# Kernel tuning notes

Measured on AMD Instinct MI355X. Metric: run time of the kernel, lower is better.

Reference implementation:

```python
import jax, jax.numpy as jnp
import numpy as np

H = 16          # head_num
DH = 64         # h_size = all_head_size // head_num
HIDDEN = 1024
ALL_HEAD = 1024
B, S = 4, 2048
NEG = -1000000000.0


def setup_inputs() -> dict:
    key = jax.random.key(0)
    ks = jax.random.split(key, 8)
    x = jax.random.normal(ks[0], (B, S, HIDDEN), dtype=jnp.float32)
    y = jax.random.normal(ks[1], (B, S, HIDDEN), dtype=jnp.float32)
    attention_mask = jax.random.randint(ks[2], (B, 1, S, S), 0, 2, dtype=jnp.int32)
    sc = 1.0 / np.sqrt(HIDDEN)
    Wq = jax.random.normal(ks[3], (HIDDEN, ALL_HEAD), dtype=jnp.float32) * sc
    Wk = jax.random.normal(ks[4], (HIDDEN, ALL_HEAD), dtype=jnp.float32) * sc
    Wv = jax.random.normal(ks[5], (HIDDEN, ALL_HEAD), dtype=jnp.float32) * sc
    Wo = jax.random.normal(ks[6], (ALL_HEAD, HIDDEN), dtype=jnp.float32) * (1.0 / np.sqrt(ALL_HEAD))
    bo = jnp.zeros((HIDDEN,), dtype=jnp.float32)
    return {"x": x, "y": y, "Wq": Wq, "Wk": Wk, "Wv": Wv, "Wo": Wo, "bo": bo,
            "attention_mask": attention_mask}


def reference(x, y, Wq, Wk, Wv, Wo, bo, attention_mask):
    b = x.shape[0]
    # projections, split heads: [B, H, S, Dh]
    q = (x @ Wq).reshape(b, -1, H, DH).transpose(0, 2, 1, 3)
    k = (x @ Wk).reshape(b, -1, H, DH).transpose(0, 2, 1, 3)
    v = (y @ Wv).reshape(b, -1, H, DH).transpose(0, 2, 1, 3)
    mask = attention_mask == 0  # True => masked (matches .eq(0))
    scores = jnp.einsum('bhqd,bhkd->bhqk', q, k)
    scores = jnp.where(mask, NEG, scores)  # masked_fill BEFORE scaling, as in source
    attn = jax.nn.softmax(scores / np.sqrt(DH), axis=-1)
    ctx = jnp.einsum('bhqk,bhkd->bhqd', attn, v)
    ctx = ctx.transpose(0, 2, 1, 3).reshape(b, -1, H * DH)
    return ctx @ Wo + bo  # dropout p=0.0 is identity
```

## Files before the change

### kernel.cpp

```cpp
#include <hip/hip_runtime.h>
#include <hip/hip_bf16.h>
#include <stdint.h>

typedef __attribute__((ext_vector_type(8))) short short8;
typedef __attribute__((ext_vector_type(4))) float f32x4;
typedef __attribute__((ext_vector_type(16))) float f32x16;
typedef __hip_bfloat16 bf16;

typedef __attribute__((address_space(3))) uint32_t lds_u32_t;
typedef __attribute__((address_space(1))) const uint32_t glb_u32_t;

__device__ __forceinline__ void gload_lds16(const void* g, void* l) {
  __builtin_amdgcn_global_load_lds((glb_u32_t*)g, (lds_u32_t*)l, 16, 0, 0);
}

__device__ __forceinline__ uint32_t cvt_pk_bf16(float lo, float hi_) {
  uint32_t r;
  asm volatile("v_cvt_pk_bf16_f32 %0, %1, %2" : "=v"(r) : "v"(lo), "v"(hi_));
  return r;
}

__device__ __forceinline__ void plane32swap(uint32_t &a, uint32_t &b) {
  auto r = __builtin_amdgcn_permlane32_swap((int)a, (int)b, false, false);
  a = (uint32_t)r[0]; b = (uint32_t)r[1];
}


__global__ void conv_bf16(const float* __restrict__ in, bf16* __restrict__ outp, int n4) {
  int i = blockIdx.x * blockDim.x + threadIdx.x;
  if (i >= n4) return;
  const float4 v = ((const float4*)in)[i];
  union { ushort4 u; bf16 h[4]; } o;
  o.h[0] = __float2bfloat16(v.x); o.h[1] = __float2bfloat16(v.y);
  o.h[2] = __float2bfloat16(v.z); o.h[3] = __float2bfloat16(v.w);
  ((ushort4*)outp)[i] = o.u;
}

__global__ void transpose_w(const float* __restrict__ W0, const float* __restrict__ W1,
                            const float* __restrict__ W2, const float* __restrict__ W3,
                            bf16* __restrict__ outp) {
  const float* W = blockIdx.z == 0 ? W0 : blockIdx.z == 1 ? W1 : blockIdx.z == 2 ? W2 : W3;
  bf16* o = outp + (size_t)blockIdx.z * 1048576;
  __shared__ float t[32][33];
  int x = threadIdx.x, y0 = threadIdx.y;
  int c0 = blockIdx.x * 32, r0 = blockIdx.y * 32;
#pragma unroll
  for (int i = 0; i < 4; i++)
    t[y0 + i*8][x] = W[(size_t)(r0 + y0 + i*8)*1024 + c0 + x];
  __syncthreads();
#pragma unroll
  for (int i = 0; i < 4; i++)
    o[(size_t)(c0 + y0 + i*8)*1024 + r0 + x] = __float2bfloat16(t[x][y0 + i*8]);
}

__global__ void maskpack(const int* __restrict__ mask, unsigned long long* __restrict__ mbits) {
  int tid = threadIdx.x;
  int lane = tid & 63, wid = tid >> 6;
  size_t word = (size_t)blockIdx.x * 4 + wid;
  int v = mask[word * 64 + lane];
  unsigned long long bits = __ballot(v == 0);
  if (lane == 0) mbits[word] = bits;
}

template<int MODE>
__global__ void gemm_bt(const bf16* __restrict__ A, const bf16* __restrict__ Bt,
                        void* __restrict__ Out, const float* __restrict__ bias) {
  const int tid = threadIdx.x;
  const int lane = tid & 63, wid = tid >> 6;
  const int g = lane >> 4, c = lane & 15;
  const int m0 = blockIdx.x * 128, n0 = blockIdx.y * 128;
  const int wm = wid >> 1, wn = wid & 1;
  __shared__ bf16 As[128 * 64];
  __shared__ bf16 Bs[128 * 64];
  f32x4 acc[4][4] = {};
  for (int k0 = 0; k0 < 1024; k0 += 64) {
#pragma unroll
    for (int i = 0; i < 4; i++) {
      int chunk = wid * 4 + i;
      int idx = chunk * 64 + lane;
      int row = idx >> 3, u = idx & 7;
      int koff = k0 + ((u ^ (row & 7)) * 8);
      gload_lds16(A  + (size_t)(m0 + row) * 1024 + koff, As + chunk * 512);
      gload_lds16(Bt + (size_t)(n0 + row) * 1024 + koff, Bs + chunk * 512);
    }
    __syncthreads();
#pragma unroll
    for (int kk = 0; kk < 2; kk++) {
      short8 af[4], bf_[4];
#pragma unroll
      for (int f = 0; f < 4; f++) {
        int ra = wm * 64 + f * 16 + c;
        af[f]  = *(const short8*)(As + ra * 64 + (((kk * 4 + g) ^ (ra & 7)) * 8));
        int rb = wn * 64 + f * 16 + c;
        bf_[f] = *(const short8*)(Bs + rb * 64 + (((kk * 4 + g) ^ (rb & 7)) * 8));
      }
#pragma unroll
      for (int fm = 0; fm < 4; fm++)
#pragma unroll
        for (int fn = 0; fn < 4; fn++)
          acc[fm][fn] = __builtin_amdgcn_mfma_f32_16x16x32_bf16(af[fm], bf_[fn], acc[fm][fn], 0, 0, 0);
    }
    __syncthreads();
  }
#pragma unroll
  for (int fm = 0; fm < 4; fm++) {
#pragma unroll
    for (int fn = 0; fn < 4; fn++) {
      int gn = n0 + wn * 64 + fn * 16 + c;
#pragma unroll
      for (int r = 0; r < 4; r++) {
        int gm = m0 + wm * 64 + fm * 16 + g * 4 + r;
        float v = acc[fm][fn][r];
        if constexpr (MODE == 2) {
          ((float*)Out)[(size_t)gm * 1024 + gn] = v + bias[gn];
        } else if constexpr (MODE == 0) {
          int b = gm >> 11, s = gm & 2047, hh = gn >> 6, d = gn & 63;
          ((bf16*)Out)[(((size_t)b * 16 + hh) * 2048 + s) * 64 + d] = __float2bfloat16(v);
        } else {
          int b = gm >> 11, s = gm & 2047, hh = gn >> 6, d = gn & 63;
          ((bf16*)Out)[(((size_t)b * 16 + hh) * 64 + d) * 2048 + s] = __float2bfloat16(v);
        }
      }
    }
  }
}

__global__ __launch_bounds__(256, 4) void attn_kernel(
    const bf16* __restrict__ Qb, const bf16* __restrict__ Kb, const bf16* __restrict__ Vt,
    const unsigned long long* __restrict__ mbits, bf16* __restrict__ ctx) {
  const int tid = threadIdx.x;
  const int lane = tid & 63, wid = tid >> 6;
  const int c5 = lane & 31, hi = lane >> 5;
  const int sid = blockIdx.x;
  const int xcd = sid & 7, idx = sid >> 3;
  const int bh = xcd * 8 + (idx >> 4);
  const int qb0 = (idx & 15) * 128 + wid * 32;
  const int b = bh >> 4, h = bh & 15;
  __shared__ bf16 Ks[2][64 * 64];
  __shared__ bf16 Vs[3][64 * 64];
  const bf16* Qp = Qb + (size_t)bh * 2048 * 64;
  const bf16* Kp = Kb + (size_t)bh * 2048 * 64;
  const bf16* Vp = Vt + (size_t)bh * 64 * 2048;
  const unsigned long long* mrow = mbits + ((size_t)b * 2048 + qb0 + c5) * 32;

  auto stage_k = [&](int kt, int sk) {
#pragma unroll
    for (int i = 0; i < 2; i++) {
      int chunk = wid * 2 + i;
      int idx2 = chunk * 64 + lane;
      int row = idx2 >> 3, u = idx2 & 7;
      gload_lds16(Kp + (size_t)(kt * 64 + row) * 64 + ((u ^ (row & 7)) * 8), &Ks[sk][chunk * 512]);
    }
  };
  auto stage_v = [&](int kt, int sv) {
#pragma unroll
    for (int i = 0; i < 2; i++) {
      int chunk = wid * 2 + i;
      int idx2 = chunk * 64 + lane;
      int row = idx2 >> 3, u = idx2 & 7;
      gload_lds16(Vp + (size_t)row * 2048 + kt * 64 + ((u ^ (row & 7)) * 8), &Vs[sv][chunk * 512]);
    }
  };

  short8 qf[4];
#pragma unroll
  for (int ks = 0; ks < 4; ks++)
    qf[ks] = *(const short8*)(Qp + (size_t)(qb0 + c5) * 64 + ks * 16 + hi * 8);

  f32x16 Oacc0 = {}, Oacc1 = {};
  float mrun = -3.0e38f, mc1 = 0.f, lrun = 0.f;
  short8 paP[4];

  const float C1 = 0.18033688011112042f;
  const float THRRAW = 44.36f;

  unsigned long long mwC, mwN;
  stage_k(0, 0);
  stage_v(0, 0);
  mwC = mrow[0];
  __syncthreads();

  int sv = 0, svp = 2;
  for (int kt = 0; kt < 32; kt++) {
    const int sk = kt & 1;
    const int svn = (sv == 2) ? 0 : sv + 1;
    if (kt < 31) { stage_k(kt + 1, sk ^ 1); stage_v(kt + 1, svn); }
    mwN = mrow[(kt + 1) & 31];

    f32x16 s0 = {}, s1 = {};
    __builtin_amdgcn_s_setprio(1);
#pragma unroll
    for (int ks = 0; ks < 4; ks++) {
      short8 aK0 = *(const short8*)(&Ks[sk][(c5)      * 64 + (((ks * 2 + hi) ^ (c5 & 7)) * 8)]);
      short8 aK1 = *(const short8*)(&Ks[sk][(32 + c5) * 64 + (((ks * 2 + hi) ^ (c5 & 7)) * 8)]);
      s0 = __builtin_amdgcn_mfma_f32_32x32x16_bf16(aK0, qf[ks], s0, 0, 0, 0);
      s1 = __builtin_amdgcn_mfma_f32_32x32x16_bf16(aK1, qf[ks], s1, 0, 0, 0);
    }
    if (kt > 0) {
#pragma unroll
      for (int ks = 0; ks < 4; ks++) {
        short8 bV0 = *(const short8*)(&Vs[svp][(c5)      * 64 + (((ks * 2 + hi) ^ (c5 & 7)) * 8)]);
        short8 bV1 = *(const short8*)(&Vs[svp][(32 + c5) * 64 + (((ks * 2 + hi) ^ (c5 & 7)) * 8)]);
        Oacc0 = __builtin_amdgcn_mfma_f32_32x32x16_bf16(paP[ks], bV0, Oacc0, 0, 0, 0);
        Oacc1 = __builtin_amdgcn_mfma_f32_32x32x16_bf16(paP[ks], bV1, Oacc1, 0, 0, 0);
      }
    }
    __builtin_amdgcn_s_setprio(0);
    float lmx = fmaxf(s0[0], s1[0]);
#pragma unroll
    for (int reg = 1; reg < 16; reg++)
      lmx = fmaxf(fmaxf(s0[reg], s1[reg]), lmx);
    if (__any(lmx > mrun + THRRAW)) {
      float rmx = fmaxf(lmx, __shfl_xor(lmx, 32));
      float mnew = fmaxf(mrun, rmx);
      float sc = exp2f((mrun - mnew) * C1);
      mrun = mnew; mc1 = mnew * C1;
      lrun *= sc;
#pragma unroll
      for (int reg = 0; reg < 16; reg++) {
        const int qrow = (reg & 3) + 8 * (reg >> 2) + 4 * hi;
        float srow = __shfl(sc, qrow);
        Oacc0[reg] *= srow; Oacc1[reg] *= srow;
      }
    }
    const uint32_t nlo = ~(((uint32_t)mwC)         >> (4 * hi));
    const uint32_t nhi = ~(((uint32_t)(mwC >> 32)) >> (4 * hi));
    uint32_t pk0[8], pk1[8];
    float lsum = 0.f;
#pragma unroll
    for (int r8 = 0; r8 < 8; r8++) {
      const int rA = 2 * r8, rB = 2 * r8 + 1;
      const int pA = (rA & 3) + 8 * (rA >> 2), pB = (rB & 3) + 8 * (rB >> 2);
      float a0 = exp2f(fmaf(s0[rA], C1, -mc1));
      float a1 = exp2f(fmaf(s0[rB], C1, -mc1));
      float b0 = exp2f(fmaf(s1[rA], C1, -mc1));
      float b1 = exp2f(fmaf(s1[rB], C1, -mc1));
      a0 = __uint_as_float(__float_as_uint(a0) & (uint32_t)(((int32_t)(nlo << (31 - pA))) >> 31));
      a1 = __uint_as_float(__float_as_uint(a1) & (uint32_t)(((int32_t)(nlo << (31 - pB))) >> 31));
      b0 = __uint_as_float(__float_as_uint(b0) & (uint32_t)(((int32_t)(nhi << (31 - pA))) >> 31));
      b1 = __uint_as_float(__float_as_uint(b1) & (uint32_t)(((int32_t)(nhi << (31 - pB))) >> 31));
      lsum += (a0 + a1) + (b0 + b1);
      pk0[r8] = cvt_pk_bf16(a0, a1);
      pk1[r8] = cvt_pk_bf16(b0, b1);
    }
    lrun += lsum;
#pragma unroll
    for (int ks = 0; ks < 4; ks++) {
      const int e0 = 2 * ((2 * ks) & 3);
      const int e1 = 2 * ((2 * ks + 1) & 3);
      uint32_t w0, w1, w2, w3;
      if (ks < 2) { w0 = pk0[e0];     w2 = pk0[e1];
                    w1 = pk0[e0 + 1]; w3 = pk0[e1 + 1]; }
      else        { w0 = pk1[e0];     w2 = pk1[e1];
                    w1 = pk1[e0 + 1]; w3 = pk1[e1 + 1]; }
      plane32swap(w0, w2);
      plane32swap(w1, w3);
      union { uint32_t u[4]; short8 s; } pu;
      pu.u[0] = w0; pu.u[1] = w1; pu.u[2] = w2; pu.u[3] = w3;
      paP[ks] = pu.s;
    }
    mwC = mwN;
    svp = sv; sv = svn;
    __syncthreads();
  }
#pragma unroll
  for (int ks = 0; ks < 4; ks++) {
    short8 bV0 = *(const short8*)(&Vs[svp][(c5)      * 64 + (((ks * 2 + hi) ^ (c5 & 7)) * 8)]);
    short8 bV1 = *(const short8*)(&Vs[svp][(32 + c5) * 64 + (((ks * 2 + hi) ^ (c5 & 7)) * 8)]);
    Oacc0 = __builtin_amdgcn_mfma_f32_32x32x16_bf16(paP[ks], bV0, Oacc0, 0, 0, 0);
    Oacc1 = __builtin_amdgcn_mfma_f32_32x32x16_bf16(paP[ks], bV1, Oacc1, 0, 0, 0);
  }
  float lfull = lrun + __shfl_xor(lrun, 32);
#pragma unroll
  for (int reg = 0; reg < 16; reg++) {
    const int qrow = (reg & 3) + 8 * (reg >> 2) + 4 * hi;
    float linv = __builtin_amdgcn_rcpf(__shfl(lfull, qrow));
    size_t base = ((size_t)b * 2048 + qb0 + qrow) * 1024 + h * 64;
    ctx[base + c5]      = __float2bfloat16(Oacc0[reg] * linv);
    ctx[base + 32 + c5] = __float2bfloat16(Oacc1[reg] * linv);
  }
}


extern "C" void kernel_launch(void* const* d_in, const int* in_sizes, int n_in,
                              void* d_out, int out_size, void* d_ws, size_t ws_size,
                              hipStream_t stream) {
  const float* x  = (const float*)d_in[0];
  const float* y  = (const float*)d_in[1];
  const float* Wq = (const float*)d_in[2];
  const float* Wk = (const float*)d_in[3];
  const float* Wv = (const float*)d_in[4];
  const float* Wo = (const float*)d_in[5];
  const float* bo = (const float*)d_in[6];
  const int* amask = (const int*)d_in[7];
  float* out = (float*)d_out;

  char* ws = (char*)d_ws;
  bf16* xb = (bf16*)ws;
  bf16* yb = (bf16*)(ws + 16777216);
  bf16* WT = (bf16*)(ws + 33554432);
  bf16* Qb = (bf16*)(ws + 41943040);
  bf16* Kb = (bf16*)(ws + 58720256);
  bf16* Vt = (bf16*)(ws + 75497472);
  unsigned long long* mbits = (unsigned long long*)(ws + 92274688);
  bf16* ctx = xb;

  conv_bf16<<<8192, 256, 0, stream>>>(x, xb, 2097152);
  conv_bf16<<<8192, 256, 0, stream>>>(y, yb, 2097152);
  transpose_w<<<dim3(32, 32, 4), dim3(32, 8), 0, stream>>>(Wq, Wk, Wv, Wo, WT);
  maskpack<<<65536, 256, 0, stream>>>(amask, mbits);

  dim3 gg(64, 8);
  gemm_bt<0><<<gg, 256, 0, stream>>>(xb, WT + 0 * 1048576, Qb, nullptr);
  gemm_bt<0><<<gg, 256, 0, stream>>>(xb, WT + 1 * 1048576, Kb, nullptr);
  gemm_bt<1><<<gg, 256, 0, stream>>>(yb, WT + 2 * 1048576, Vt, nullptr);

  attn_kernel<<<1024, 256, 0, stream>>>(Qb, Kb, Vt, mbits, ctx);

  gemm_bt<2><<<gg, 256, 0, stream>>>(ctx, WT + 3 * 1048576, out, bo);
}
```

Baseline: 285.9 us.

## Merge conversion and Q/K projection launches, use native exp2 and bitfield masks

Fuses the two fp32-to-bf16 conversion launches into one 2D-grid launch and merges the Q and K projection GEMMs into one launch with 16 column panels (MODE 3), where the upper half offsets the weight and output pointers. This cuts launch count and lets Q/K blocks fill the GPU together. In the attention kernel, exp2f is replaced by the raw hardware exp2 builtin, and the mask-bit extraction shift pair by a signed bitfield extract. The raw exp2 drops denormal/range handling, which should be harmless for softmax.

```diff
diff --git a/kernel.cpp b/kernel.cpp
--- a/kernel.cpp
+++ b/kernel.cpp
@@ -26,9 +26,12 @@
 }
 
 
-__global__ void conv_bf16(const float* __restrict__ in, bf16* __restrict__ outp, int n4) {
+__global__ void conv_bf16(const float* __restrict__ inx, const float* __restrict__ iny,
+                          bf16* __restrict__ ox, bf16* __restrict__ oy, int n4) {
   int i = blockIdx.x * blockDim.x + threadIdx.x;
   if (i >= n4) return;
+  const float* in = blockIdx.y ? iny : inx;
+  bf16* outp = blockIdx.y ? oy : ox;
   const float4 v = ((const float4*)in)[i];
   union { ushort4 u; bf16 h[4]; } o;
   o.h[0] = __float2bfloat16(v.x); o.h[1] = __float2bfloat16(v.y);
@@ -68,7 +71,14 @@
   const int tid = threadIdx.x;
   const int lane = tid & 63, wid = tid >> 6;
   const int g = lane >> 4, c = lane & 15;
-  const int m0 = blockIdx.x * 128, n0 = blockIdx.y * 128;
+  const int m0 = blockIdx.x * 128;
+  const int npanel = (MODE == 3) ? (blockIdx.y & 7) : blockIdx.y;
+  const int n0 = npanel * 128;
+  const bf16* BtE = Bt;
+  bf16* OE = (bf16*)Out;
+  if constexpr (MODE == 3) {
+    if (blockIdx.y >= 8) { BtE += 1048576; OE += 8388608; }
+  }
   const int wm = wid >> 1, wn = wid & 1;
   __shared__ bf16 As[128 * 64];
   __shared__ bf16 Bs[128 * 64];
@@ -80,8 +90,8 @@
       int idx = chunk * 64 + lane;
       int row = idx >> 3, u = idx & 7;
       int koff = k0 + ((u ^ (row & 7)) * 8);
-      gload_lds16(A  + (size_t)(m0 + row) * 1024 + koff, As + chunk * 512);
-      gload_lds16(Bt + (size_t)(n0 + row) * 1024 + koff, Bs + chunk * 512);
+      gload_lds16(A   + (size_t)(m0 + row) * 1024 + koff, As + chunk * 512);
+      gload_lds16(BtE + (size_t)(n0 + row) * 1024 + koff, Bs + chunk * 512);
     }
     __syncthreads();
 #pragma unroll
@@ -113,9 +123,9 @@
         float v = acc[fm][fn][r];
         if constexpr (MODE == 2) {
           ((float*)Out)[(size_t)gm * 1024 + gn] = v + bias[gn];
-        } else if constexpr (MODE == 0) {
+        } else if constexpr (MODE == 0 || MODE == 3) {
           int b = gm >> 11, s = gm & 2047, hh = gn >> 6, d = gn & 63;
-          ((bf16*)Out)[(((size_t)b * 16 + hh) * 2048 + s) * 64 + d] = __float2bfloat16(v);
+          OE[(((size_t)b * 16 + hh) * 2048 + s) * 64 + d] = __float2bfloat16(v);
         } else {
           int b = gm >> 11, s = gm & 2047, hh = gn >> 6, d = gn & 63;
           ((bf16*)Out)[(((size_t)b * 16 + hh) * 64 + d) * 2048 + s] = __float2bfloat16(v);
@@ -213,7 +223,7 @@
     if (__any(lmx > mrun + THRRAW)) {
       float rmx = fmaxf(lmx, __shfl_xor(lmx, 32));
       float mnew = fmaxf(mrun, rmx);
-      float sc = exp2f((mrun - mnew) * C1);
+      float sc = __builtin_amdgcn_exp2f((mrun - mnew) * C1);
       mrun = mnew; mc1 = mnew * C1;
       lrun *= sc;
 #pragma unroll
@@ -231,14 +241,14 @@
     for (int r8 = 0; r8 < 8; r8++) {
       const int rA = 2 * r8, rB = 2 * r8 + 1;
       const int pA = (rA & 3) + 8 * (rA >> 2), pB = (rB & 3) + 8 * (rB >> 2);
-      float a0 = exp2f(fmaf(s0[rA], C1, -mc1));
-      float a1 = exp2f(fmaf(s0[rB], C1, -mc1));
-      float b0 = exp2f(fmaf(s1[rA], C1, -mc1));
-      float b1 = exp2f(fmaf(s1[rB], C1, -mc1));
-      a0 = __uint_as_float(__float_as_uint(a0) & (uint32_t)(((int32_t)(nlo << (31 - pA))) >> 31));
-      a1 = __uint_as_float(__float_as_uint(a1) & (uint32_t)(((int32_t)(nlo << (31 - pB))) >> 31));
-      b0 = __uint_as_float(__float_as_uint(b0) & (uint32_t)(((int32_t)(nhi << (31 - pA))) >> 31));
-      b1 = __uint_as_float(__float_as_uint(b1) & (uint32_t)(((int32_t)(nhi << (31 - pB))) >> 31));
+      float a0 = __builtin_amdgcn_exp2f(fmaf(s0[rA], C1, -mc1));
+      float a1 = __builtin_amdgcn_exp2f(fmaf(s0[rB], C1, -mc1));
+      float b0 = __builtin_amdgcn_exp2f(fmaf(s1[rA], C1, -mc1));
+      float b1 = __builtin_amdgcn_exp2f(fmaf(s1[rB], C1, -mc1));
+      a0 = __uint_as_float(__float_as_uint(a0) & (uint32_t)__builtin_amdgcn_sbfe(nlo, pA, 1));
+      a1 = __uint_as_float(__float_as_uint(a1) & (uint32_t)__builtin_amdgcn_sbfe(nlo, pB, 1));
+      b0 = __uint_as_float(__float_as_uint(b0) & (uint32_t)__builtin_amdgcn_sbfe(nhi, pA, 1));
+      b1 = __uint_as_float(__float_as_uint(b1) & (uint32_t)__builtin_amdgcn_sbfe(nhi, pB, 1));
       lsum += (a0 + a1) + (b0 + b1);
       pk0[r8] = cvt_pk_bf16(a0, a1);
       pk1[r8] = cvt_pk_bf16(b0, b1);
@@ -305,17 +315,14 @@
   unsigned long long* mbits = (unsigned long long*)(ws + 92274688);
   bf16* ctx = xb;
 
-  conv_bf16<<<8192, 256, 0, stream>>>(x, xb, 2097152);
-  conv_bf16<<<8192, 256, 0, stream>>>(y, yb, 2097152);
+  conv_bf16<<<dim3(8192, 2), 256, 0, stream>>>(x, y, xb, yb, 2097152);
   transpose_w<<<dim3(32, 32, 4), dim3(32, 8), 0, stream>>>(Wq, Wk, Wv, Wo, WT);
   maskpack<<<65536, 256, 0, stream>>>(amask, mbits);
 
-  dim3 gg(64, 8);
-  gemm_bt<0><<<gg, 256, 0, stream>>>(xb, WT + 0 * 1048576, Qb, nullptr);
-  gemm_bt<0><<<gg, 256, 0, stream>>>(xb, WT + 1 * 1048576, Kb, nullptr);
-  gemm_bt<1><<<gg, 256, 0, stream>>>(yb, WT + 2 * 1048576, Vt, nullptr);
+  gemm_bt<3><<<dim3(64, 16), 256, 0, stream>>>(xb, WT, Qb, nullptr);
+  gemm_bt<1><<<dim3(64, 8),  256, 0, stream>>>(yb, WT + 2 * 1048576, Vt, nullptr);
 
   attn_kernel<<<1024, 256, 0, stream>>>(Qb, Kb, Vt, mbits, ctx);
 
-  gemm_bt<2><<<gg, 256, 0, stream>>>(ctx, WT + 3 * 1048576, out, bo);
-}
+  gemm_bt<2><<<dim3(64, 8), 256, 0, stream>>>(ctx, WT + 3 * 1048576, out, bo);
+}
```

Result: faster. 273.1 us (-4.5%).
